# Optimization experiments

Measured on AMD Instinct MI355X. Metric: run time of the kernel, lower is better.

## Reference

```python
import jax, jax.numpy as jnp
import numpy as np

N_HEADS = 16
LN_EPS = 1e-6


def _mha(q_in, kv_in, mask, wq, bq, wk, bk, wv, bv, wo, bo):
    B, Sq, D = q_in.shape
    H = N_HEADS
    dh = D // H
    def split(x):  # [B,S,D] -> [B,H,S,dh]
        return x.reshape(B, -1, H, dh).transpose(0, 2, 1, 3)
    q = split(q_in @ wq + bq)
    k = split(kv_in @ wk + bk)
    v = split(kv_in @ wv + bv)
    scores = jnp.einsum('bhqd,bhkd->bhqk', q, k) / jnp.sqrt(jnp.asarray(dh, q.dtype))
    scores = scores + mask * (-1e9)
    attn = jax.nn.softmax(scores, axis=-1)
    out = jnp.einsum('bhqk,bhkd->bhqd', attn, v)
    out = out.transpose(0, 2, 1, 3).reshape(B, Sq, D)
    return out @ wo + bo


def _layer_norm(x, gamma, beta):
    mu = jnp.mean(x, axis=-1, keepdims=True)
    var = jnp.mean(jnp.square(x - mu), axis=-1, keepdims=True)
    return (x - mu) * jax.lax.rsqrt(var + LN_EPS) * gamma + beta


def setup_inputs() -> dict:
    key = jax.random.key(0)
    B, S_dec, S_enc, D, F = 4, 1024, 1024, 1024, 4096
    ks = jax.random.split(key, 16)
    s = 0.02
    inp = {
        'inputs': jax.random.normal(ks[0], (B, S_dec, D), jnp.float32),
        'enc_outputs': jax.random.normal(ks[1], (B, S_enc, D), jnp.float32),
        # causal look-ahead mask: 1 above diagonal -> -1e9 added to scores
        'mask_1': jnp.triu(jnp.ones((S_dec, S_dec), jnp.float32), k=1)[None, None],
        'mask_2': jnp.zeros((B, 1, 1, S_enc), jnp.float32),
    }
    names = ['wq1', 'wk1', 'wv1', 'wo1', 'wq2', 'wk2', 'wv2', 'wo2']
    for i, n in enumerate(names):
        inp[n] = jax.random.normal(ks[2 + i], (D, D), jnp.float32) * s
        inp['b' + n[1:]] = jnp.zeros((D,), jnp.float32)
    inp['w_ff1'] = jax.random.normal(ks[10], (D, F), jnp.float32) * s
    inp['b_ff1'] = jnp.zeros((F,), jnp.float32)
    inp['w_ff2'] = jax.random.normal(ks[11], (F, D), jnp.float32) * s
    inp['b_ff2'] = jnp.zeros((D,), jnp.float32)
    for i in (1, 2, 3):
        inp[f'g{i}'] = jnp.ones((D,), jnp.float32)
        inp[f'beta{i}'] = jnp.zeros((D,), jnp.float32)
    return inp


def reference(inputs, enc_outputs, mask_1, mask_2,
              wq1, bq1, wk1, bk1, wv1, bv1, wo1, bo1,
              wq2, bq2, wk2, bk2, wv2, bv2, wo2, bo2,
              w_ff1, b_ff1, w_ff2, b_ff2,
              g1, beta1, g2, beta2, g3, beta3):
    # causal self-attention + residual + LN (dropout inactive at inference)
    attn = _mha(inputs, inputs, mask_1, wq1, bq1, wk1, bk1, wv1, bv1, wo1, bo1)
    attn = _layer_norm(attn + inputs, g1, beta1)
    # encoder-decoder cross-attention + residual + LN
    attn2 = _mha(attn, enc_outputs, mask_2, wq2, bq2, wk2, bk2, wv2, bv2, wo2, bo2)
    attn2 = _layer_norm(attn2 + attn, g2, beta2)
    # FFN + residual + LN
    h = jax.nn.relu(attn2 @ w_ff1 + b_ff1)
    h = h @ w_ff2 + b_ff2
    return _layer_norm(h + attn2, g3, beta3)
```

## Files before the change

### kernel.cpp

```cpp
#include <hip/hip_runtime.h>
#include <stdint.h>

typedef unsigned short ushort_t;
typedef __attribute__((ext_vector_type(8))) short bf16x8;
typedef __attribute__((ext_vector_type(4))) float f32x4;
typedef __attribute__((ext_vector_type(4))) unsigned short us4;

#define DEV __device__ __forceinline__

DEV unsigned short f2bf(float f) {
  union { float f; unsigned u; } x; x.f = f;
  unsigned r = x.u + 0x7fffu + ((x.u >> 16) & 1u);
  return (unsigned short)(r >> 16);
}

DEV float bf2f(unsigned short u) {
  union { unsigned u; float f; } x; x.u = (unsigned)u << 16; return x.f;
}

DEV uint2 pk4(float v0, float v1, float v2, float v3) {
  unsigned d0, d1;
  asm("v_cvt_pk_bf16_f32 %0, %1, %2" : "=v"(d0) : "v"(v0), "v"(v1));
  asm("v_cvt_pk_bf16_f32 %0, %1, %2" : "=v"(d1) : "v"(v2), "v"(v3));
  uint2 r; r.x = d0; r.y = d1; return r;
}

DEV void gload16(const void* g, void* l) {
  __builtin_amdgcn_global_load_lds(
      (const __attribute__((address_space(1))) unsigned int*)g,
      (__attribute__((address_space(3))) unsigned int*)l, 16, 0, 0);
}

#define MFMA16 __builtin_amdgcn_mfma_f32_16x16x32_bf16

__global__ __launch_bounds__(256) void cast_bf16_kernel(
    const float* __restrict__ x, ushort_t* __restrict__ y, int n4) {
  int i = blockIdx.x * 256 + threadIdx.x;
  if (i >= n4) return;
  float4 v = ((const float4*)x)[i];
  us4 o; o.x = f2bf(v.x); o.y = f2bf(v.y); o.z = f2bf(v.z); o.w = f2bf(v.w);
  ((us4*)y)[i] = o;
}

__global__ __launch_bounds__(256) void reduce_cast_kernel(
    const ushort_t* __restrict__ p0, const ushort_t* __restrict__ p1,
    ushort_t* __restrict__ y, int n4) {
  int i = blockIdx.x * 256 + threadIdx.x;
  if (i >= n4) return;
  us4 a = ((const us4*)p0)[i];
  us4 b = ((const us4*)p1)[i];
  us4 o;
  o.x = f2bf(bf2f(a.x) + bf2f(b.x));
  o.y = f2bf(bf2f(a.y) + bf2f(b.y));
  o.z = f2bf(bf2f(a.z) + bf2f(b.z));
  o.w = f2bf(bf2f(a.w) + bf2f(b.w));
  ((us4*)y)[i] = o;
}

__global__ __launch_bounds__(256) void transpose_cast_kernel(
    const float* __restrict__ W, ushort_t* __restrict__ dst, int K, int N) {
  __shared__ float tile[64][65];
  int n0 = blockIdx.x * 64, k0 = blockIdx.y * 64;
  int tid = threadIdx.x;
#pragma unroll
  for (int it = 0; it < 16; ++it) {
    int idx = it * 256 + tid; int r = idx >> 6, c = idx & 63;
    tile[r][c] = W[(size_t)(k0 + r) * N + n0 + c];
  }
  __syncthreads();
#pragma unroll
  for (int it = 0; it < 16; ++it) {
    int idx = it * 256 + tid; int r = idx >> 6, c = idx & 63;
    dst[(size_t)(n0 + r) * K + k0 + c] = f2bf(tile[c][r]);
  }
}

struct Src8 { const float* p[8]; };
__global__ __launch_bounds__(256) void transpose_cast8_kernel(
    Src8 s, ushort_t* __restrict__ dst) {
  __shared__ float tile[64][65];
  const float* W = s.p[blockIdx.z];
  ushort_t* out = dst + (size_t)blockIdx.z * 1048576;
  int n0 = blockIdx.x * 64, k0 = blockIdx.y * 64;
  int tid = threadIdx.x;
#pragma unroll
  for (int it = 0; it < 16; ++it) {
    int idx = it * 256 + tid; int r = idx >> 6, c = idx & 63;
    tile[r][c] = W[(size_t)(k0 + r) * 1024 + n0 + c];
  }
  __syncthreads();
#pragma unroll
  for (int it = 0; it < 16; ++it) {
    int idx = it * 256 + tid; int r = idx >> 6, c = idx & 63;
    out[(size_t)(n0 + r) * 1024 + k0 + c] = f2bf(tile[c][r]);
  }
}

__global__ __launch_bounds__(256) void transpose_v_kernel(
    const ushort_t* __restrict__ V, int ldv, ushort_t* __restrict__ vT) {
  __shared__ ushort_t tile[64][65];
  int s0 = blockIdx.x * 64;
  int bh = blockIdx.y;
  int b = bh >> 4, h = bh & 15;
  int tid = threadIdx.x;
#pragma unroll
  for (int it = 0; it < 4; ++it) {
    int idx = it * 256 + tid; int r = idx >> 4, c = (idx & 15) * 4;
    us4 v = *(const us4*)&V[(size_t)(b * 1024 + s0 + r) * ldv + h * 64 + c];
    tile[r][c] = v.x; tile[r][c + 1] = v.y; tile[r][c + 2] = v.z; tile[r][c + 3] = v.w;
  }
  __syncthreads();
#pragma unroll
  for (int it = 0; it < 4; ++it) {
    int idx = it * 256 + tid; int r = idx >> 4, c = (idx & 15) * 4;
    us4 o; o.x = tile[c][r]; o.y = tile[c + 1][r]; o.z = tile[c + 2][r]; o.w = tile[c + 3][r];
    *(us4*)&vT[((size_t)bh * 64 + r) * 1024 + s0 + c] = o;
  }
}

template <int RELU>
__global__ __launch_bounds__(256, 2) void gemm_bt(
    const ushort_t* __restrict__ A, const ushort_t* __restrict__ Bt,
    const float* __restrict__ b0, const float* __restrict__ b1,
    const float* __restrict__ b2, const float* __restrict__ b3,
    ushort_t* __restrict__ Cb, int M, int N, int K, int Ks, long long pstr) {
  __shared__ ushort_t sA[4096];
  __shared__ ushort_t sB[4096];
  const int tid = threadIdx.x;
  const int w = tid >> 6, lane = tid & 63;
  const int lrow = lane & 15, lk = lane >> 4;
  const int m0 = blockIdx.x * 128, n0 = blockIdx.y * 128;
  const int kz = blockIdx.z * Ks;
  const int wr = w >> 1, wc = w & 1;
  f32x4 acc[4][4] = {};
  const int brow0 = (w * 1024 + lane * 16) >> 6;
  const int kbyte = (lane * 16) & 63;

  for (int kt = kz; kt < kz + Ks; kt += 32) {
    __syncthreads();
    const ushort_t* ga = A + (size_t)(m0 + brow0) * K + kt + (kbyte >> 1);
    gload16(ga, (char*)sA + w * 1024);
    gload16(ga + (size_t)64 * K, (char*)sA + 4096 + w * 1024);
    const ushort_t* gb = Bt + (size_t)(n0 + brow0) * K + kt + (kbyte >> 1);
    gload16(gb, (char*)sB + w * 1024);
    gload16(gb + (size_t)64 * K, (char*)sB + 4096 + w * 1024);
    __syncthreads();
    bf16x8 aF[4], bF[4];
#pragma unroll
    for (int t = 0; t < 4; ++t) {
      bF[t] = *(const bf16x8*)((const char*)sB + ((wc * 64 + t * 16 + lrow) << 6) + (lk << 4));
      aF[t] = *(const bf16x8*)((const char*)sA + ((wr * 64 + t * 16 + lrow) << 6) + (lk << 4));
    }
#pragma unroll
    for (int mt = 0; mt < 4; ++mt)
#pragma unroll
      for (int nt = 0; nt < 4; ++nt)
        acc[mt][nt] = MFMA16(bF[nt], aF[mt], acc[mt][nt], 0, 0, 0);
  }
  ushort_t* Cbz = Cb + (long long)blockIdx.z * pstr;
#pragma unroll
  for (int nt = 0; nt < 4; ++nt) {
    int colb = n0 + wc * 64 + nt * 16 + lk * 4;
    int seg = colb >> 10;
    const float* bp = seg == 0 ? b0 : seg == 1 ? b1 : seg == 2 ? b2 : b3;
    float4 bv = *(const float4*)(bp + (colb & 1023));
    if (blockIdx.z != 0) { bv.x = bv.y = bv.z = bv.w = 0.f; }
#pragma unroll
    for (int mt = 0; mt < 4; ++mt) {
      int row = m0 + wr * 64 + mt * 16 + lrow;
      float v0 = acc[mt][nt][0] + bv.x, v1 = acc[mt][nt][1] + bv.y;
      float v2 = acc[mt][nt][2] + bv.z, v3 = acc[mt][nt][3] + bv.w;
      if (RELU) {
        v0 = fmaxf(v0, 0.f); v1 = fmaxf(v1, 0.f);
        v2 = fmaxf(v2, 0.f); v3 = fmaxf(v3, 0.f);
      }
      *(uint2*)&Cbz[(size_t)row * N + colb] = pk4(v0, v1, v2, v3);
    }
  }
}

template <int RELU>
__global__ __launch_bounds__(512, 1) void gemm256(
    const ushort_t* __restrict__ A, const ushort_t* __restrict__ Bt,
    const float* __restrict__ b0, const float* __restrict__ b1,
    const float* __restrict__ b2, const float* __restrict__ b3,
    ushort_t* __restrict__ Cb, int M, int N, int K, int Ks, long long pstr) {
  extern __shared__ char L[];
  const int tid = threadIdx.x;
  const int w = tid >> 6, lane = tid & 63;
  const int lrow = lane & 15, lk = lane >> 4;
  const int wm = w >> 2, wn = w & 3;
  const int m0 = blockIdx.x * 256, n0 = blockIdx.y * 256;
  const int kz = blockIdx.z * Ks;
  const int nt = Ks >> 6;

  const int srow = w * 8 + (lane >> 3);
  const int gsw = (lane & 7) ^ ((lane >> 3) & 7);
  const ushort_t* srcA = A + (size_t)(m0 + srow) * K + kz + gsw * 8;
  const ushort_t* srcB = Bt + (size_t)(n0 + srow) * K + kz + gsw * 8;
  const int dstw = w * 1024;

#define STG2(M_, T_, S_)                                                     \
  do {                                                                       \
    const ushort_t* g0 = ((M_) ? srcB : srcA) + (size_t)(T_) * 64 +          \
                         (size_t)(S_) * 64 * K;                              \
    char* d_ = L + (((T_) & 1) << 16) + ((M_) << 15) + (S_) * 8192 + dstw;   \
    gload16(g0, d_);                                                         \
    gload16(g0 + (size_t)64 * K, d_ + 8192);                                 \
  } while (0)

  f32x4 acc[8][4] = {};
  const int swz = (lrow & 7) << 4;
  const int k0b = (lk << 4) ^ swz;
  const int k1b = (64 + (lk << 4)) ^ swz;
  const int aBase = (wm * 128 + lrow) << 7;
  const int bBase = ((wn * 64 + lrow) << 7) + 32768;

  STG2(0, 0, 0); STG2(0, 0, 2); STG2(1, 0, 0); STG2(1, 0, 2);
  STG2(0, 1, 0); STG2(0, 1, 2);
  asm volatile("s_waitcnt vmcnt(4)" ::: "memory");
  __builtin_amdgcn_s_barrier();

  for (int t = 0; t < nt; ++t) {
    const int buf = (t & 1) << 16;
    const char* base = L + buf;
    bf16x8 aF[8], bF0, bF1;
    {
      bF0 = *(const bf16x8*)(base + bBase + k0b);
      bF1 = *(const bf16x8*)(base + bBase + 2048 + k0b);
#pragma unroll
      for (int m = 0; m < 8; ++m) aF[m] = *(const bf16x8*)(base + aBase + m * 2048 + k0b);
      if (t + 1 < nt) STG2(1, t + 1, 0);
      __builtin_amdgcn_s_barrier();
      __builtin_amdgcn_s_setprio(1);
#pragma unroll
      for (int m = 0; m < 8; ++m) {
        acc[m][0] = MFMA16(bF0, aF[m], acc[m][0], 0, 0, 0);
        acc[m][1] = MFMA16(bF1, aF[m], acc[m][1], 0, 0, 0);
      }
      __builtin_amdgcn_s_setprio(0);
      __builtin_amdgcn_s_barrier();
    }
    {
      bF0 = *(const bf16x8*)(base + bBase + 4096 + k0b);
      bF1 = *(const bf16x8*)(base + bBase + 6144 + k0b);
      if (t + 1 < nt) STG2(1, t + 1, 2);
      __builtin_amdgcn_s_barrier();
      __builtin_amdgcn_s_setprio(1);
#pragma unroll
      for (int m = 0; m < 8; ++m) {
        acc[m][2] = MFMA16(bF0, aF[m], acc[m][2], 0, 0, 0);
        acc[m][3] = MFMA16(bF1, aF[m], acc[m][3], 0, 0, 0);
      }
      __builtin_amdgcn_s_setprio(0);
      __builtin_amdgcn_s_barrier();
    }
    {
      bF0 = *(const bf16x8*)(base + bBase + k1b);
      bF1 = *(const bf16x8*)(base + bBase + 2048 + k1b);
#pragma unroll
      for (int m = 0; m < 8; ++m) aF[m] = *(const bf16x8*)(base + aBase + m * 2048 + k1b);
      __builtin_amdgcn_s_barrier();
      __builtin_amdgcn_s_setprio(1);
#pragma unroll
      for (int m = 0; m < 8; ++m) {
        acc[m][0] = MFMA16(bF0, aF[m], acc[m][0], 0, 0, 0);
        acc[m][1] = MFMA16(bF1, aF[m], acc[m][1], 0, 0, 0);
      }
      __builtin_amdgcn_s_setprio(0);
      __builtin_amdgcn_s_barrier();
    }
    {
      bF0 = *(const bf16x8*)(base + bBase + 4096 + k1b);
      bF1 = *(const bf16x8*)(base + bBase + 6144 + k1b);
      if (t + 2 < nt) {
        STG2(0, t + 2, 0); STG2(0, t + 2, 2);
        asm volatile("s_waitcnt vmcnt(4)" ::: "memory");
      } else {
        asm volatile("s_waitcnt vmcnt(0)" ::: "memory");
      }
      __builtin_amdgcn_s_barrier();
      __builtin_amdgcn_s_setprio(1);
#pragma unroll
      for (int m = 0; m < 8; ++m) {
        acc[m][2] = MFMA16(bF0, aF[m], acc[m][2], 0, 0, 0);
        acc[m][3] = MFMA16(bF1, aF[m], acc[m][3], 0, 0, 0);
      }
      __builtin_amdgcn_s_setprio(0);
      __builtin_amdgcn_s_barrier();
    }
  }
#undef STG2

  ushort_t* Cbz = Cb + (long long)blockIdx.z * pstr;
#pragma unroll
  for (int n = 0; n < 4; ++n) {
    int colb = n0 + wn * 64 + n * 16 + lk * 4;
    int seg = colb >> 10;
    const float* bp = seg == 0 ? b0 : seg == 1 ? b1 : seg == 2 ? b2 : b3;
    float4 bv = *(const float4*)(bp + (colb & 1023));
    if (blockIdx.z != 0) { bv.x = bv.y = bv.z = bv.w = 0.f; }
#pragma unroll
    for (int m = 0; m < 8; ++m) {
      int row = m0 + wm * 128 + m * 16 + lrow;
      float v0 = acc[m][n][0] + bv.x, v1 = acc[m][n][1] + bv.y;
      float v2 = acc[m][n][2] + bv.z, v3 = acc[m][n][3] + bv.w;
      if (RELU) {
        v0 = fmaxf(v0, 0.f); v1 = fmaxf(v1, 0.f);
        v2 = fmaxf(v2, 0.f); v3 = fmaxf(v3, 0.f);
      }
      *(uint2*)&Cbz[(size_t)row * N + colb] = pk4(v0, v1, v2, v3);
    }
  }
}

template <int CAUSAL>
__global__ __launch_bounds__(256, 3) void attn_kernel(
    const ushort_t* __restrict__ Q, int ldq,
    const ushort_t* __restrict__ Kp, int ldk,
    const ushort_t* __restrict__ vT,
    const float* __restrict__ mask2,
    ushort_t* __restrict__ O) {
  __shared__ ushort_t sK[2][4096];
  __shared__ ushort_t sV[2][4096];
  __shared__ ushort_t sP[4][2048];
  const int bh = blockIdx.x, qb = blockIdx.y;
  const int b = bh >> 4, h = bh & 15;
  const int tid = threadIdx.x, w = tid >> 6, lane = tid & 63;
  const int lrow = lane & 15, lk = lane >> 4;
  const int q0 = qb * 128 + w * 32;

  bf16x8 qF[2][2];
#pragma unroll
  for (int g = 0; g < 2; ++g) {
    const ushort_t* qptr =
        Q + (size_t)(b * 1024 + q0 + g * 16 + lrow) * ldq + h * 64 + lk * 8;
    qF[g][0] = *(const bf16x8*)qptr;
    qF[g][1] = *(const bf16x8*)(qptr + 32);
  }
  f32x4 oacc[2][4] = {};
  float m_[2] = {-3.0e38f, -3.0e38f}, l_[2] = {0.f, 0.f};
  const int nkb = CAUSAL ? (qb * 2 + 2) : 16;
  const float C = 0.18033688011112042f;

  const int sr = w * 16 + (lane >> 3);
  const int scb = (((lane & 7) ^ (lane >> 3)) * 16);
  const ushort_t* kbase = Kp + (size_t)(b * 1024 + sr) * ldk + h * 64 + (scb >> 1);
  const ushort_t* vbase = vT + ((size_t)bh * 64 + sr) * 1024 + (scb >> 1);
  char* dstK0 = (char*)sK[0] + w * 2048;
  char* dstV0 = (char*)sV[0] + w * 2048;

#define STAGE(kb_, bufi)                                              \
  do {                                                                \
    const ushort_t* gk = kbase + (size_t)(kb_) * 64 * ldk;            \
    gload16(gk, dstK0 + (bufi) * 8192);                               \
    gload16(gk + (size_t)8 * ldk, dstK0 + (bufi) * 8192 + 1024);      \
    const ushort_t* gv = vbase + (kb_) * 64;                          \
    gload16(gv, dstV0 + (bufi) * 8192);                               \
    gload16(gv + (size_t)8 * 1024, dstV0 + (bufi) * 8192 + 1024);     \
  } while (0)

  STAGE(0, 0);
  const int swz = (lrow & 7) << 4;

  for (int kb = 0; kb < nkb; ++kb) {
    const int buf = kb & 1;
    __syncthreads();
    if (kb + 1 < nkb) STAGE(kb + 1, buf ^ 1);

    const char* kB = (const char*)sK[buf];
    const char* vB = (const char*)sV[buf];
    bool skip[2], edge[2];
#pragma unroll
    for (int g = 0; g < 2; ++g) {
      int qming = q0 + g * 16;
      skip[g] = CAUSAL && (kb * 64 > qming + 15);
      edge[g] = CAUSAL && !skip[g] && (kb * 64 + 63 > qming);
    }
    f32x4 sc[2][4];
    __builtin_amdgcn_s_setprio(1);
#pragma unroll
    for (int kt = 0; kt < 4; ++kt) {
      const char* rp = kB + ((kt * 16 + lrow) << 7);
      bf16x8 k0 = *(const bf16x8*)(rp + ((lk * 16) ^ swz));
      bf16x8 k1 = *(const bf16x8*)(rp + ((64 + lk * 16) ^ swz));
      f32x4 z0 = {};
      z0 = MFMA16(k0, qF[0][0], z0, 0, 0, 0);
      sc[0][kt] = MFMA16(k1, qF[0][1], z0, 0, 0, 0);
      f32x4 z1 = {};
      z1 = MFMA16(k0, qF[1][0], z1, 0, 0, 0);
      sc[1][kt] = MFMA16(k1, qF[1][1], z1, 0, 0, 0);
    }
    __builtin_amdgcn_s_setprio(0);
    float4 mv[4];
    if (!CAUSAL) {
#pragma unroll
      for (int kt = 0; kt < 4; ++kt)
        mv[kt] = *(const float4*)&mask2[b * 1024 + kb * 64 + kt * 16 + lk * 4];
    }
#pragma unroll
    for (int g = 0; g < 2; ++g) {
      if (skip[g]) continue;
      if (CAUSAL) {
        if (edge[g]) {
          int qrel = q0 + g * 16 + lrow - kb * 64;
#pragma unroll
          for (int kt = 0; kt < 4; ++kt)
#pragma unroll
            for (int j = 0; j < 4; ++j)
              if (kt * 16 + lk * 4 + j > qrel) sc[g][kt][j] = -3.0e38f;
        }
      } else {
#pragma unroll
        for (int kt = 0; kt < 4; ++kt) {
          sc[g][kt][0] = fmaf(mv[kt].x, -8e9f, sc[g][kt][0]);
          sc[g][kt][1] = fmaf(mv[kt].y, -8e9f, sc[g][kt][1]);
          sc[g][kt][2] = fmaf(mv[kt].z, -8e9f, sc[g][kt][2]);
          sc[g][kt][3] = fmaf(mv[kt].w, -8e9f, sc[g][kt][3]);
        }
      }
      float pmax = fmaxf(
          fmaxf(fmaxf(sc[g][0][0], sc[g][0][1]), fmaxf(sc[g][0][2], sc[g][0][3])),
          fmaxf(fmaxf(sc[g][1][0], sc[g][1][1]), fmaxf(sc[g][1][2], sc[g][1][3])));
      pmax = fmaxf(pmax, fmaxf(
          fmaxf(fmaxf(sc[g][2][0], sc[g][2][1]), fmaxf(sc[g][2][2], sc[g][2][3])),
          fmaxf(fmaxf(sc[g][3][0], sc[g][3][1]), fmaxf(sc[g][3][2], sc[g][3][3]))));
      pmax = fmaxf(pmax, __shfl_xor(pmax, 16));
      pmax = fmaxf(pmax, __shfl_xor(pmax, 32));
      if (__any(pmax - m_[g] > 64.f)) {
        float mnew = fmaxf(m_[g], pmax);
        float scale = __builtin_exp2f((m_[g] - mnew) * C);
        l_[g] *= scale;
        m_[g] = mnew;
#pragma unroll
        for (int t = 0; t < 4; ++t) {
          oacc[g][t][0] *= scale; oacc[g][t][1] *= scale;
          oacc[g][t][2] *= scale; oacc[g][t][3] *= scale;
        }
      }
      const float mC = m_[g] * C;
      float ps = 0.f;
#pragma unroll
      for (int kt = 0; kt < 4; ++kt)
#pragma unroll
        for (int j = 0; j < 4; ++j) {
          float e = __builtin_exp2f(fmaf(sc[g][kt][j], C, -mC));
          sc[g][kt][j] = e;
          ps += e;
        }
      ps += __shfl_xor(ps, 16);
      ps += __shfl_xor(ps, 32);
      l_[g] += ps;
      char* bp = (char*)sP[w] + (g * 16 + lrow) * 128;
#pragma unroll
      for (int kt = 0; kt < 4; ++kt) {
        uint2 dd = pk4(sc[g][kt][0], sc[g][kt][1], sc[g][kt][2], sc[g][kt][3]);
        *(uint2*)(bp + ((kt * 32 + lk * 8) ^ swz)) = dd;
      }
    }
    bf16x8 pF[2][2];
#pragma unroll
    for (int g = 0; g < 2; ++g) {
      if (skip[g]) continue;
      const char* pB = (const char*)sP[w] + (g * 16 + lrow) * 128;
      pF[g][0] = *(const bf16x8*)(pB + ((lk * 16) ^ swz));
      pF[g][1] = *(const bf16x8*)(pB + ((64 + lk * 16) ^ swz));
    }
    __builtin_amdgcn_s_setprio(1);
#pragma unroll
    for (int t = 0; t < 4; ++t) {
      const char* rp = vB + ((t * 16 + lrow) << 7);
      bf16x8 v0 = *(const bf16x8*)(rp + ((lk * 16) ^ swz));
      bf16x8 v1 = *(const bf16x8*)(rp + ((64 + lk * 16) ^ swz));
      if (!skip[0]) {
        oacc[0][t] = MFMA16(v0, pF[0][0], oacc[0][t], 0, 0, 0);
        oacc[0][t] = MFMA16(v1, pF[0][1], oacc[0][t], 0, 0, 0);
      }
      if (!skip[1]) {
        oacc[1][t] = MFMA16(v0, pF[1][0], oacc[1][t], 0, 0, 0);
        oacc[1][t] = MFMA16(v1, pF[1][1], oacc[1][t], 0, 0, 0);
      }
    }
    __builtin_amdgcn_s_setprio(0);
  }
#undef STAGE
#pragma unroll
  for (int g = 0; g < 2; ++g) {
    float invl = 1.f / l_[g];
    int row = q0 + g * 16 + lrow;
    ushort_t* op = O + (size_t)(b * 1024 + row) * 1024 + h * 64;
#pragma unroll
    for (int t = 0; t < 4; ++t) {
      uint2 dd = pk4(oacc[g][t][0] * invl, oacc[g][t][1] * invl,
                     oacc[g][t][2] * invl, oacc[g][t][3] * invl);
      *(uint2*)&op[t * 16 + lk * 4] = dd;
    }
  }
}

template <int RESBF, int NPART, int WF32>
__global__ __launch_bounds__(256) void ln_kernel(
    const ushort_t* __restrict__ p0, const ushort_t* __restrict__ p1,
    const ushort_t* __restrict__ p2, const ushort_t* __restrict__ p3,
    const void* __restrict__ rp,
    const float* __restrict__ g, const float* __restrict__ be,
    float* __restrict__ yf, ushort_t* __restrict__ yb) {
  int row = blockIdx.x, tid = threadIdx.x;
  size_t off = (size_t)row * 1024 + tid * 4;
  us4 a = *(const us4*)(p0 + off);
  float x0 = bf2f(a.x), x1 = bf2f(a.y), x2 = bf2f(a.z), x3 = bf2f(a.w);
  if (NPART >= 2) {
    us4 t = *(const us4*)(p1 + off);
    x0 += bf2f(t.x); x1 += bf2f(t.y); x2 += bf2f(t.z); x3 += bf2f(t.w);
  }
  if (NPART >= 4) {
    us4 t2 = *(const us4*)(p2 + off);
    us4 t3 = *(const us4*)(p3 + off);
    x0 += bf2f(t2.x) + bf2f(t3.x); x1 += bf2f(t2.y) + bf2f(t3.y);
    x2 += bf2f(t2.z) + bf2f(t3.z); x3 += bf2f(t2.w) + bf2f(t3.w);
  }
  if (RESBF) {
    us4 r = *(const us4*)((const ushort_t*)rp + off);
    x0 += bf2f(r.x); x1 += bf2f(r.y); x2 += bf2f(r.z); x3 += bf2f(r.w);
  } else {
    float4 r = *(const float4*)((const float*)rp + off);
    x0 += r.x; x1 += r.y; x2 += r.z; x3 += r.w;
  }
  float s = x0 + x1 + x2 + x3;
  float s2 = x0 * x0 + x1 * x1 + x2 * x2 + x3 * x3;
#pragma unroll
  for (int o = 1; o < 64; o <<= 1) { s += __shfl_xor(s, o); s2 += __shfl_xor(s2, o); }
  __shared__ float sh[8];
  if ((tid & 63) == 0) { sh[tid >> 6] = s; sh[4 + (tid >> 6)] = s2; }
  __syncthreads();
  s = sh[0] + sh[1] + sh[2] + sh[3];
  s2 = sh[4] + sh[5] + sh[6] + sh[7];
  float mu = s * 0.0009765625f;
  float var = s2 * 0.0009765625f - mu * mu;
  float inv = rsqrtf(var + 1e-6f);
  float4 gv = *(const float4*)(g + tid * 4);
  float4 bv = *(const float4*)(be + tid * 4);
  float y0 = (x0 - mu) * inv * gv.x + bv.x;
  float y1 = (x1 - mu) * inv * gv.y + bv.y;
  float y2 = (x2 - mu) * inv * gv.z + bv.z;
  float y3 = (x3 - mu) * inv * gv.w + bv.w;
  if (WF32) {
    *(float4*)(yf + off) = make_float4(y0, y1, y2, y3);
  } else {
    us4 o; o.x = f2bf(y0); o.y = f2bf(y1); o.z = f2bf(y2); o.w = f2bf(y3);
    *(us4*)(yb + off) = o;
  }
}

extern "C" void kernel_launch(void* const* d_in, const int* in_sizes, int n_in,
                              void* d_out, int out_size, void* d_ws, size_t ws_size,
                              hipStream_t stream) {
  (void)in_sizes; (void)n_in; (void)out_size; (void)ws_size;
  const float* inputs = (const float*)d_in[0];
  const float* enc    = (const float*)d_in[1];
  const float* mask2  = (const float*)d_in[3];
  const float* wq1 = (const float*)d_in[4];  const float* bq1 = (const float*)d_in[5];
  const float* wk1 = (const float*)d_in[6];  const float* bk1 = (const float*)d_in[7];
  const float* wv1 = (const float*)d_in[8];  const float* bv1 = (const float*)d_in[9];
  const float* wo1 = (const float*)d_in[10]; const float* bo1 = (const float*)d_in[11];
  const float* wq2 = (const float*)d_in[12]; const float* bq2 = (const float*)d_in[13];
  const float* wk2 = (const float*)d_in[14]; const float* bk2 = (const float*)d_in[15];
  const float* wv2 = (const float*)d_in[16]; const float* bv2 = (const float*)d_in[17];
  const float* wo2 = (const float*)d_in[18]; const float* bo2 = (const float*)d_in[19];
  const float* wff1 = (const float*)d_in[20]; const float* bff1 = (const float*)d_in[21];
  const float* wff2 = (const float*)d_in[22]; const float* bff2 = (const float*)d_in[23];
  const float* g1 = (const float*)d_in[24]; const float* be1 = (const float*)d_in[25];
  const float* g2 = (const float*)d_in[26]; const float* be2 = (const float*)d_in[27];
  const float* g3 = (const float*)d_in[28]; const float* be3 = (const float*)d_in[29];

  char* ws = (char*)d_ws;
  const size_t MB = 1024 * 1024;
  const size_t W1M = 1048576;
  ushort_t* wt    = (ushort_t*)ws;
  ushort_t* xb    = (ushort_t*)(ws + 32 * MB);
  ushort_t* encb  = (ushort_t*)(ws + 40 * MB);
  ushort_t* qkvb  = (ushort_t*)(ws + 48 * MB);
  ushort_t* vtb   = (ushort_t*)(ws + 72 * MB);
  ushort_t* attnb = (ushort_t*)(ws + 80 * MB);
  ushort_t* y1b   = (ushort_t*)(ws + 88 * MB);
  ushort_t* y2b   = (ushort_t*)(ws + 96 * MB);
  ushort_t* cp    = (ushort_t*)(ws + 104 * MB);
  ushort_t* q2b   = (ushort_t*)(ws + 32 * MB);
  ushort_t* kv2b  = (ushort_t*)(ws + 56 * MB);
  ushort_t* hb    = (ushort_t*)(ws + 32 * MB);
  ushort_t* pp    = (ushort_t*)(ws + 104 * MB);
  float* outf = (float*)d_out;
  const long long PE = 4LL * 1024 * 1024;

  cast_bf16_kernel<<<4096, 256, 0, stream>>>(inputs, xb, 1048576);
  cast_bf16_kernel<<<4096, 256, 0, stream>>>(enc, encb, 1048576);
  Src8 s8; s8.p[0] = wq1; s8.p[1] = wk1; s8.p[2] = wv1; s8.p[3] = wo1;
           s8.p[4] = wq2; s8.p[5] = wk2; s8.p[6] = wv2; s8.p[7] = wo2;
  transpose_cast8_kernel<<<dim3(16, 16, 8), 256, 0, stream>>>(s8, wt);
  transpose_cast_kernel<<<dim3(64, 16), 256, 0, stream>>>(wff1, wt + 8 * W1M, 1024, 4096);
  transpose_cast_kernel<<<dim3(16, 64), 256, 0, stream>>>(wff2, wt + 12 * W1M, 4096, 1024);

  gemm256<0><<<dim3(16, 12, 1), 512, 131072, stream>>>(
      xb, wt, bq1, bk1, bv1, bv1, qkvb, 4096, 3072, 1024, 1024, 0);
  transpose_v_kernel<<<dim3(16, 64), 256, 0, stream>>>(qkvb + 2048, 3072, vtb);
  attn_kernel<1><<<dim3(64, 8), 256, 0, stream>>>(
      qkvb, 3072, qkvb + 1024, 3072, vtb, nullptr, attnb);
  gemm_bt<0><<<dim3(32, 8, 2), 256, 0, stream>>>(
      attnb, wt + 3 * W1M, bo1, bo1, bo1, bo1, cp, 4096, 1024, 1024, 512, PE);
  ln_kernel<0, 2, 0><<<4096, 256, 0, stream>>>(cp, cp + PE, nullptr, nullptr,
                                               inputs, g1, be1, nullptr, y1b);

  gemm_bt<0><<<dim3(32, 8, 2), 256, 0, stream>>>(
      y1b, wt + 4 * W1M, bq2, bq2, bq2, bq2, cp, 4096, 1024, 1024, 512, PE);
  reduce_cast_kernel<<<4096, 256, 0, stream>>>(cp, cp + PE, q2b, 1048576);
  gemm_bt<0><<<dim3(32, 16, 1), 256, 0, stream>>>(
      encb, wt + 5 * W1M, bk2, bv2, bk2, bk2, kv2b, 4096, 2048, 1024, 1024, 0);
  transpose_v_kernel<<<dim3(16, 64), 256, 0, stream>>>(kv2b + 1024, 2048, vtb);
  attn_kernel<0><<<dim3(64, 8), 256, 0, stream>>>(
      q2b, 1024, kv2b, 2048, vtb, mask2, attnb);
  gemm_bt<0><<<dim3(32, 8, 2), 256, 0, stream>>>(
      attnb, wt + 7 * W1M, bo2, bo2, bo2, bo2, cp, 4096, 1024, 1024, 512, PE);
  ln_kernel<1, 2, 0><<<4096, 256, 0, stream>>>(cp, cp + PE, nullptr, nullptr,
                                               y1b, g2, be2, nullptr, y2b);

  gemm256<1><<<dim3(16, 16, 1), 512, 131072, stream>>>(
      y2b, wt + 8 * W1M, bff1, bff1 + 1024, bff1 + 2048, bff1 + 3072,
      hb, 4096, 4096, 1024, 1024, 0);
  gemm256<0><<<dim3(16, 4, 4), 512, 131072, stream>>>(
      hb, wt + 12 * W1M, bff2, bff2, bff2, bff2, pp, 4096, 1024, 4096, 1024, PE);
  ln_kernel<1, 4, 1><<<4096, 256, 0, stream>>>(pp, pp + PE, pp + 2 * PE, pp + 3 * PE,
                                               y2b, g3, be3, outf, nullptr);
}
```

Before: 360.4 us.

## Load attention K/V fragments directly from global into registers, drop LDS staging

The attention kernel no longer stages K and V tiles through double-buffered shared memory with block-wide barriers. Each wave now loads its K fragments straight from global memory into registers, prefetching the next tile into a ping-pong register set, and loads V fragments per tile. This removes the LDS traffic and the per-iteration __syncthreads. In exchange, every wave re-reads the same K/V from global/L2 (four times the global traffic per block), uses more registers, and the occupancy hint drops from 3 to 2 blocks. The loop is unrolled by two and assumes nkb is even, which holds for both the causal and cross-attention configurations.

```diff
diff --git a/kernel.cpp b/kernel.cpp
--- a/kernel.cpp
+++ b/kernel.cpp
@@ -315,14 +315,12 @@
 }
 
 template <int CAUSAL>
-__global__ __launch_bounds__(256, 3) void attn_kernel(
+__global__ __launch_bounds__(256, 2) void attn_kernel(
     const ushort_t* __restrict__ Q, int ldq,
     const ushort_t* __restrict__ Kp, int ldk,
     const ushort_t* __restrict__ vT,
     const float* __restrict__ mask2,
     ushort_t* __restrict__ O) {
-  __shared__ ushort_t sK[2][4096];
-  __shared__ ushort_t sV[2][4096];
   __shared__ ushort_t sP[4][2048];
   const int bh = blockIdx.x, qb = blockIdx.y;
   const int b = bh >> 4, h = bh & 15;
@@ -342,54 +340,43 @@
   float m_[2] = {-3.0e38f, -3.0e38f}, l_[2] = {0.f, 0.f};
   const int nkb = CAUSAL ? (qb * 2 + 2) : 16;
   const float C = 0.18033688011112042f;
-
-  const int sr = w * 16 + (lane >> 3);
-  const int scb = (((lane & 7) ^ (lane >> 3)) * 16);
-  const ushort_t* kbase = Kp + (size_t)(b * 1024 + sr) * ldk + h * 64 + (scb >> 1);
-  const ushort_t* vbase = vT + ((size_t)bh * 64 + sr) * 1024 + (scb >> 1);
-  char* dstK0 = (char*)sK[0] + w * 2048;
-  char* dstV0 = (char*)sV[0] + w * 2048;
-
-#define STAGE(kb_, bufi)                                              \
-  do {                                                                \
-    const ushort_t* gk = kbase + (size_t)(kb_) * 64 * ldk;            \
-    gload16(gk, dstK0 + (bufi) * 8192);                               \
-    gload16(gk + (size_t)8 * ldk, dstK0 + (bufi) * 8192 + 1024);      \
-    const ushort_t* gv = vbase + (kb_) * 64;                          \
-    gload16(gv, dstV0 + (bufi) * 8192);                               \
-    gload16(gv + (size_t)8 * 1024, dstV0 + (bufi) * 8192 + 1024);     \
-  } while (0)
-
-  STAGE(0, 0);
   const int swz = (lrow & 7) << 4;
 
-  for (int kb = 0; kb < nkb; ++kb) {
-    const int buf = kb & 1;
-    __syncthreads();
-    if (kb + 1 < nkb) STAGE(kb + 1, buf ^ 1);
-
-    const char* kB = (const char*)sK[buf];
-    const char* vB = (const char*)sV[buf];
-    bool skip[2], edge[2];
-#pragma unroll
-    for (int g = 0; g < 2; ++g) {
-      int qming = q0 + g * 16;
-      skip[g] = CAUSAL && (kb * 64 > qming + 15);
-      edge[g] = CAUSAL && !skip[g] && (kb * 64 + 63 > qming);
+  const ushort_t* kbase = Kp + ((size_t)(b * 1024) + lrow) * ldk + h * 64 + lk * 8;
+  const ushort_t* vbase = vT + ((size_t)bh * 64 + lrow) * 1024 + lk * 8;
+
+  auto ldkf = [&](int kb_, bf16x8* kf) {
+    const ushort_t* p = kbase + (size_t)kb_ * 64 * ldk;
+#pragma unroll
+    for (int kt = 0; kt < 4; ++kt) {
+      kf[2 * kt]     = *(const bf16x8*)(p + (size_t)kt * 16 * ldk);
+      kf[2 * kt + 1] = *(const bf16x8*)(p + (size_t)kt * 16 * ldk + 32);
+    }
+  };
+
+  auto tile = [&](const bf16x8* kf, bf16x8* kn, int kb) {
+    const bool sk0 = CAUSAL && (kb * 64 > q0 + 15);
+    const bool sk1 = CAUSAL && (kb * 64 > q0 + 31);
+    if (kb + 1 < nkb) ldkf(kb + 1, kn);
+    bf16x8 vf[8];
+    if (!(sk0 && sk1)) {
+      const ushort_t* vp = vbase + kb * 64;
+#pragma unroll
+      for (int t = 0; t < 4; ++t) {
+        vf[2 * t]     = *(const bf16x8*)(vp + (size_t)t * 16384);
+        vf[2 * t + 1] = *(const bf16x8*)(vp + (size_t)t * 16384 + 32);
+      }
     }
     f32x4 sc[2][4];
     __builtin_amdgcn_s_setprio(1);
 #pragma unroll
     for (int kt = 0; kt < 4; ++kt) {
-      const char* rp = kB + ((kt * 16 + lrow) << 7);
-      bf16x8 k0 = *(const bf16x8*)(rp + ((lk * 16) ^ swz));
-      bf16x8 k1 = *(const bf16x8*)(rp + ((64 + lk * 16) ^ swz));
       f32x4 z0 = {};
-      z0 = MFMA16(k0, qF[0][0], z0, 0, 0, 0);
-      sc[0][kt] = MFMA16(k1, qF[0][1], z0, 0, 0, 0);
+      z0 = MFMA16(kf[2 * kt], qF[0][0], z0, 0, 0, 0);
+      sc[0][kt] = MFMA16(kf[2 * kt + 1], qF[0][1], z0, 0, 0, 0);
       f32x4 z1 = {};
-      z1 = MFMA16(k0, qF[1][0], z1, 0, 0, 0);
-      sc[1][kt] = MFMA16(k1, qF[1][1], z1, 0, 0, 0);
+      z1 = MFMA16(kf[2 * kt], qF[1][0], z1, 0, 0, 0);
+      sc[1][kt] = MFMA16(kf[2 * kt + 1], qF[1][1], z1, 0, 0, 0);
     }
     __builtin_amdgcn_s_setprio(0);
     float4 mv[4];
@@ -400,9 +387,9 @@
     }
 #pragma unroll
     for (int g = 0; g < 2; ++g) {
-      if (skip[g]) continue;
+      if (g == 0 ? sk0 : sk1) continue;
       if (CAUSAL) {
-        if (edge[g]) {
+        if (kb * 64 + 63 > q0 + g * 16) {
           int qrel = q0 + g * 16 + lrow - kb * 64;
 #pragma unroll
           for (int kt = 0; kt < 4; ++kt)
@@ -461,7 +448,7 @@
     bf16x8 pF[2][2];
 #pragma unroll
     for (int g = 0; g < 2; ++g) {
-      if (skip[g]) continue;
+      if (g == 0 ? sk0 : sk1) continue;
       const char* pB = (const char*)sP[w] + (g * 16 + lrow) * 128;
       pF[g][0] = *(const bf16x8*)(pB + ((lk * 16) ^ swz));
       pF[g][1] = *(const bf16x8*)(pB + ((64 + lk * 16) ^ swz));
@@ -469,21 +456,25 @@
     __builtin_amdgcn_s_setprio(1);
 #pragma unroll
     for (int t = 0; t < 4; ++t) {
-      const char* rp = vB + ((t * 16 + lrow) << 7);
-      bf16x8 v0 = *(const bf16x8*)(rp + ((lk * 16) ^ swz));
-      bf16x8 v1 = *(const bf16x8*)(rp + ((64 + lk * 16) ^ swz));
-      if (!skip[0]) {
-        oacc[0][t] = MFMA16(v0, pF[0][0], oacc[0][t], 0, 0, 0);
-        oacc[0][t] = MFMA16(v1, pF[0][1], oacc[0][t], 0, 0, 0);
-      }
-      if (!skip[1]) {
-        oacc[1][t] = MFMA16(v0, pF[1][0], oacc[1][t], 0, 0, 0);
-        oacc[1][t] = MFMA16(v1, pF[1][1], oacc[1][t], 0, 0, 0);
+      if (!sk0) {
+        oacc[0][t] = MFMA16(vf[2 * t], pF[0][0], oacc[0][t], 0, 0, 0);
+        oacc[0][t] = MFMA16(vf[2 * t + 1], pF[0][1], oacc[0][t], 0, 0, 0);
+      }
+      if (!sk1) {
+        oacc[1][t] = MFMA16(vf[2 * t], pF[1][0], oacc[1][t], 0, 0, 0);
+        oacc[1][t] = MFMA16(vf[2 * t + 1], pF[1][1], oacc[1][t], 0, 0, 0);
       }
     }
     __builtin_amdgcn_s_setprio(0);
-  }
-#undef STAGE
+  };
+
+  bf16x8 kfA[8], kfB[8];
+  ldkf(0, kfA);
+  for (int kb = 0; kb < nkb; kb += 2) {
+    tile(kfA, kfB, kb);
+    tile(kfB, kfA, kb + 1);
+  }
+
 #pragma unroll
   for (int g = 0; g < 2; ++g) {
     float invl = 1.f / l_[g];
```

Result: slower. 396.1 us (+9.9%).

## Simplify GEMM main loop to one barrier per k-tile with double buffering

Applied to the files above, without the earlier changes.

Replaces the four-phase ping-pong schedule, which had eight barriers per 64-wide k-tile and staggered A/B prefetch two tiles ahead, with a simpler double-buffered loop. Each iteration issues the next tile's B then A loads, does two half-k MFMA passes over all 8x4 accumulators, then waits for all outstanding loads and hits a single barrier. The aim is to cut barrier and synchronisation overhead. In exchange, prefetch depth drops to one tile and vmcnt(0) stalls at the end of every iteration, so global-load latency may be exposed.

```diff
diff --git a/kernel.cpp b/kernel.cpp
--- a/kernel.cpp
+++ b/kernel.cpp
@@ -200,13 +200,14 @@
   const ushort_t* srcB = Bt + (size_t)(n0 + srow) * K + kz + gsw * 8;
   const int dstw = w * 1024;
 
-#define STG2(M_, T_, S_)                                                     \
-  do {                                                                       \
-    const ushort_t* g0 = ((M_) ? srcB : srcA) + (size_t)(T_) * 64 +          \
-                         (size_t)(S_) * 64 * K;                              \
-    char* d_ = L + (((T_) & 1) << 16) + ((M_) << 15) + (S_) * 8192 + dstw;   \
-    gload16(g0, d_);                                                         \
-    gload16(g0 + (size_t)64 * K, d_ + 8192);                                 \
+#define STG4(M_, T_)                                                  \
+  do {                                                                \
+    const ushort_t* g0 = ((M_) ? srcB : srcA) + (size_t)(T_) * 64;    \
+    char* d_ = L + (((T_) & 1) << 16) + ((M_) << 15) + dstw;          \
+    gload16(g0, d_);                                                  \
+    gload16(g0 + (size_t)64 * K, d_ + 8192);                          \
+    gload16(g0 + (size_t)128 * K, d_ + 16384);                        \
+    gload16(g0 + (size_t)192 * K, d_ + 24576);                        \
   } while (0)
 
   f32x4 acc[8][4] = {};
@@ -216,81 +217,42 @@
   const int aBase = (wm * 128 + lrow) << 7;
   const int bBase = ((wn * 64 + lrow) << 7) + 32768;
 
-  STG2(0, 0, 0); STG2(0, 0, 2); STG2(1, 0, 0); STG2(1, 0, 2);
-  STG2(0, 1, 0); STG2(0, 1, 2);
-  asm volatile("s_waitcnt vmcnt(4)" ::: "memory");
+  STG4(0, 0); STG4(1, 0);
+  asm volatile("s_waitcnt vmcnt(0)" ::: "memory");
   __builtin_amdgcn_s_barrier();
 
   for (int t = 0; t < nt; ++t) {
-    const int buf = (t & 1) << 16;
-    const char* base = L + buf;
-    bf16x8 aF[8], bF0, bF1;
-    {
-      bF0 = *(const bf16x8*)(base + bBase + k0b);
-      bF1 = *(const bf16x8*)(base + bBase + 2048 + k0b);
-#pragma unroll
-      for (int m = 0; m < 8; ++m) aF[m] = *(const bf16x8*)(base + aBase + m * 2048 + k0b);
-      if (t + 1 < nt) STG2(1, t + 1, 0);
-      __builtin_amdgcn_s_barrier();
-      __builtin_amdgcn_s_setprio(1);
-#pragma unroll
-      for (int m = 0; m < 8; ++m) {
-        acc[m][0] = MFMA16(bF0, aF[m], acc[m][0], 0, 0, 0);
-        acc[m][1] = MFMA16(bF1, aF[m], acc[m][1], 0, 0, 0);
-      }
-      __builtin_amdgcn_s_setprio(0);
-      __builtin_amdgcn_s_barrier();
-    }
-    {
-      bF0 = *(const bf16x8*)(base + bBase + 4096 + k0b);
-      bF1 = *(const bf16x8*)(base + bBase + 6144 + k0b);
-      if (t + 1 < nt) STG2(1, t + 1, 2);
-      __builtin_amdgcn_s_barrier();
-      __builtin_amdgcn_s_setprio(1);
-#pragma unroll
-      for (int m = 0; m < 8; ++m) {
-        acc[m][2] = MFMA16(bF0, aF[m], acc[m][2], 0, 0, 0);
-        acc[m][3] = MFMA16(bF1, aF[m], acc[m][3], 0, 0, 0);
-      }
-      __builtin_amdgcn_s_setprio(0);
-      __builtin_amdgcn_s_barrier();
-    }
-    {
-      bF0 = *(const bf16x8*)(base + bBase + k1b);
-      bF1 = *(const bf16x8*)(base + bBase + 2048 + k1b);
-#pragma unroll
-      for (int m = 0; m < 8; ++m) aF[m] = *(const bf16x8*)(base + aBase + m * 2048 + k1b);
-      __builtin_amdgcn_s_barrier();
-      __builtin_amdgcn_s_setprio(1);
-#pragma unroll
-      for (int m = 0; m < 8; ++m) {
-        acc[m][0] = MFMA16(bF0, aF[m], acc[m][0], 0, 0, 0);
-        acc[m][1] = MFMA16(bF1, aF[m], acc[m][1], 0, 0, 0);
-      }
-      __builtin_amdgcn_s_setprio(0);
-      __builtin_amdgcn_s_barrier();
-    }
-    {
-      bF0 = *(const bf16x8*)(base + bBase + 4096 + k1b);
-      bF1 = *(const bf16x8*)(base + bBase + 6144 + k1b);
-      if (t + 2 < nt) {
-        STG2(0, t + 2, 0); STG2(0, t + 2, 2);
-        asm volatile("s_waitcnt vmcnt(4)" ::: "memory");
-      } else {
-        asm volatile("s_waitcnt vmcnt(0)" ::: "memory");
-      }
-      __builtin_amdgcn_s_barrier();
-      __builtin_amdgcn_s_setprio(1);
-#pragma unroll
-      for (int m = 0; m < 8; ++m) {
-        acc[m][2] = MFMA16(bF0, aF[m], acc[m][2], 0, 0, 0);
-        acc[m][3] = MFMA16(bF1, aF[m], acc[m][3], 0, 0, 0);
-      }
-      __builtin_amdgcn_s_setprio(0);
-      __builtin_amdgcn_s_barrier();
-    }
-  }
-#undef STG2
+    const char* base = L + ((t & 1) << 16);
+    bf16x8 aF[8], bF[4];
+    if (t + 1 < nt) STG4(1, t + 1);
+#pragma unroll
+    for (int n = 0; n < 4; ++n) bF[n] = *(const bf16x8*)(base + bBase + n * 2048 + k0b);
+#pragma unroll
+    for (int m = 0; m < 8; ++m) aF[m] = *(const bf16x8*)(base + aBase + m * 2048 + k0b);
+    __builtin_amdgcn_s_setprio(1);
+#pragma unroll
+    for (int m = 0; m < 8; ++m)
+#pragma unroll
+      for (int n = 0; n < 4; ++n)
+        acc[m][n] = MFMA16(bF[n], aF[m], acc[m][n], 0, 0, 0);
+    __builtin_amdgcn_s_setprio(0);
+    if (t + 1 < nt) STG4(0, t + 1);
+#pragma unroll
+    for (int n = 0; n < 4; ++n) bF[n] = *(const bf16x8*)(base + bBase + n * 2048 + k1b);
+#pragma unroll
+    for (int m = 0; m < 8; ++m) aF[m] = *(const bf16x8*)(base + aBase + m * 2048 + k1b);
+    __builtin_amdgcn_s_setprio(1);
+#pragma unroll
+    for (int m = 0; m < 8; ++m)
+#pragma unroll
+      for (int n = 0; n < 4; ++n)
+        acc[m][n] = MFMA16(bF[n], aF[m], acc[m][n], 0, 0, 0);
+    __builtin_amdgcn_s_setprio(0);
+    asm volatile("s_waitcnt lgkmcnt(0)" ::: "memory");
+    asm volatile("s_waitcnt vmcnt(0)" ::: "memory");
+    __builtin_amdgcn_s_barrier();
+  }
+#undef STG4
 
   ushort_t* Cbz = Cb + (long long)blockIdx.z * pstr;
 #pragma unroll
```

Measured after the change: 352.6 us. 2.2% less time.
